# Optimization experiments

Measured on AMD Instinct MI355X. Metric: run time of the kernel, lower is better.

The kernel has to match this reference:

```python
import jax, jax.numpy as jnp
import numpy as np

BS, T, D_IN = 128, 32, 128
DH = 128          # controller hidden size == memory word width M
N_SLOTS = 512     # memory rows
EPS = 1e-8


def _split_read(o):
    # o: [bs, M+6] -> k, beta, g, s(3), gamma
    k = o[:, :DH]
    beta = jax.nn.softplus(o[:, DH])
    g = jax.nn.sigmoid(o[:, DH + 1])
    s = jax.nn.softmax(o[:, DH + 2:DH + 5], axis=-1)
    gamma = 1.0 + jax.nn.softplus(o[:, DH + 5])
    return k, beta, g, s, gamma


def _attention(k, beta, g, s, gamma, mem, w_prev):
    # content addressing: cosine similarity sharpened by beta
    dot = jnp.einsum('bnm,bm->bn', mem, k)
    denom = jnp.linalg.norm(mem, axis=-1) * jnp.linalg.norm(k, axis=-1, keepdims=True) + EPS
    w_c = jax.nn.softmax(beta[:, None] * dot / denom, axis=-1)
    # gate interpolation with previous weights
    w_g = g[:, None] * w_c + (1.0 - g[:, None]) * w_prev
    # circular shift convolution over offsets {-1, 0, +1}
    w_t = (s[:, 0:1] * jnp.roll(w_g, -1, axis=-1)
           + s[:, 1:2] * w_g
           + s[:, 2:3] * jnp.roll(w_g, 1, axis=-1))
    # sharpening
    w = w_t ** gamma[:, None]
    return w / (jnp.sum(w, axis=-1, keepdims=True) + EPS)


def setup_inputs() -> dict:
    key = jax.random.key(0)
    ks = jax.random.split(key, 8)
    sc = lambda fan_in: 1.0 / np.sqrt(fan_in)
    return {
        'x':    jax.random.normal(ks[0], (BS, T, D_IN), jnp.float32),
        'Wxh':  jax.random.normal(ks[1], (D_IN, DH), jnp.float32) * sc(D_IN),
        'Whh':  jax.random.normal(ks[2], (DH, DH), jnp.float32) * sc(DH),
        'Wrh':  jax.random.normal(ks[3], (DH, DH), jnp.float32) * sc(DH),
        'bh':   jnp.zeros((DH,), jnp.float32),
        'Wout': jax.random.normal(ks[4], (DH + DH, D_IN), jnp.float32) * sc(2 * DH),
        'bout': jnp.zeros((D_IN,), jnp.float32),
        'Wr':   jax.random.normal(ks[5], (DH, DH + 6), jnp.float32) * sc(DH),
        'br':   jnp.zeros((DH + 6,), jnp.float32),
        'Ww':   jax.random.normal(ks[6], (DH, 3 * DH + 6), jnp.float32) * sc(DH),
        'bw':   jnp.zeros((3 * DH + 6,), jnp.float32),
    }


def reference(x, Wxh, Whh, Wrh, bh, Wout, bout, Wr, br, Ww, bw):
    bs = x.shape[0]
    h0 = jnp.zeros((bs, DH), x.dtype)
    r0 = jnp.zeros((bs, DH), x.dtype)
    w0 = jnp.full((bs, N_SLOTS), 1.0 / N_SLOTS, x.dtype)
    mem0 = jnp.full((bs, N_SLOTS, DH), 1e-6, x.dtype)

    def step(carry, x_t):
        h, r, w_prev, mem = carry
        # controller state
        h = jnp.tanh(x_t @ Wxh + h @ Whh + r @ Wrh + bh)
        # head parameter projections
        o_r = h @ Wr + br
        o_w = h @ Ww + bw
        k_r, b_r, g_r, s_r, y_r = _split_read(o_r)
        k_w, b_w_, g_w, s_w, y_w = _split_read(o_w[:, :DH + 6])
        e = jax.nn.sigmoid(o_w[:, DH + 6:2 * DH + 6])   # erase [bs, M]
        a = jnp.tanh(o_w[:, 2 * DH + 6:3 * DH + 6])     # add   [bs, M]
        # addressing (w_previous updated sequentially, read then write)
        w_r = _attention(k_r, b_r, g_r, s_r, y_r, mem, w_prev)
        w_w = _attention(k_w, b_w_, g_w, s_w, y_w, mem, w_r)
        # read
        r = jnp.einsum('bn,bnm->bm', w_r, mem)
        # erase / add write
        mem = mem * (1.0 - w_w[:, :, None] * e[:, None, :]) + w_w[:, :, None] * a[:, None, :]
        # output
        y = jnp.concatenate([h, r], axis=-1) @ Wout + bout
        return (h, r, w_w, mem), y

    _, ys = jax.lax.scan(step, (h0, r0, w0, mem0), jnp.swapaxes(x, 0, 1))
    return jnp.swapaxes(ys, 0, 1)  # [bs, ft, d_output]
```

## Files before the change

kernel.cpp:

```cpp
#include <hip/hip_runtime.h>
#include <hip/hip_bf16.h>
#include <math.h>

#define NT 1024
#define BSZ 128
#define TSTEPS 32
#define DIN 128
#define DHH 128
#define NSLOT 512
#define EPSF 1e-8f

static constexpr int F_FLOATS = 7160;
static constexpr size_t LDS_BYTES = 131072 + F_FLOATS * sizeof(float);

__device__ __forceinline__ float bf_lo(unsigned u) {
  union { unsigned u; float f; } c; c.u = u << 16; return c.f;
}
__device__ __forceinline__ float bf_hi(unsigned u) {
  union { unsigned u; float f; } c; c.u = u & 0xffff0000u; return c.f;
}
__device__ __forceinline__ unsigned short f2us(float f) {
  union { unsigned short s; __hip_bfloat16 h; } c; c.h = __float2bfloat16(f); return c.s;
}
__device__ __forceinline__ unsigned pkbf(float a, float b) {
  union { __hip_bfloat162 h2; unsigned u; } c;
  c.h2 = __float22bfloat162_rn(make_float2(a, b));
  return c.u;
}
__device__ __forceinline__ float sigmoid_(float x) { return 1.0f / (1.0f + __expf(-x)); }
__device__ __forceinline__ float softplus_(float x) {
  return fmaxf(x, 0.0f) + log1pf(__expf(-fabsf(x)));
}
__device__ __forceinline__ float tanh_(float x) {
  float e = __expf(-2.0f * fabsf(x));
  float t = (1.0f - e) / (1.0f + e);
  return copysignf(t, x);
}
__device__ __forceinline__ float waveSum(float v) {
#pragma unroll
  for (int m = 32; m >= 1; m >>= 1) v += __shfl_xor(v, m);
  return v;
}

__global__ __launch_bounds__(NT, 4)
void ntm_kernel(const float* __restrict__ x,
                const float* __restrict__ Wxh,
                const float* __restrict__ Whh,
                const float* __restrict__ Wrh,
                const float* __restrict__ bh,
                const float* __restrict__ Wout,
                const float* __restrict__ bout,
                const float* __restrict__ Wr,
                const float* __restrict__ br,
                const float* __restrict__ Ww,
                const float* __restrict__ bw,
                float* __restrict__ out)
{
  extern __shared__ char smem[];
  uint4* memv = (uint4*)smem;
  float* F = (float*)(smem + 131072);

  const int b = blockIdx.x;
  const int tid = threadIdx.x;
  const int g = tid >> 4, l = tid & 15;
  const int lane = tid & 63, wid = tid >> 6;

  float* U      = F + 0;
  float* yP     = F + 2560;
  float* sWprev = F + 4608;
  float* sWr    = F + 5120;
  float* sP1    = F + 5632;
  float* sOr    = F + 6144;
  float* sOw    = F + 6288;
  float* sH     = F + 6680;
  float* sR     = F + 6808;
  float* sXt    = F + 6936;
  float* sP     = F + 7064;
  uint4* krP    = (uint4*)(sP1 + 0);
  uint4* kwP    = (uint4*)(sP1 + 64);
  float* eR     = U + 0;
  float* eW     = U + 512;

  {
    const unsigned short mb = f2us(1e-6f);
    const unsigned w32 = ((unsigned)mb << 16) | mb;
    const uint4 fv = make_uint4(w32, w32, w32, w32);
    for (int i = tid; i < NSLOT * DHH / 8; i += NT) memv[i] = fv;
  }
  for (int i = tid; i < NSLOT; i += NT) sWprev[i] = 1.0f / NSLOT;
  if (tid < DHH) { sH[tid] = 0.0f; sR[tid] = 0.0f; }
  if (tid < DIN) sXt[tid] = x[(size_t)b * TSTEPS * DIN + tid];
  __syncthreads();

  for (int t = 0; t < TSTEPS; ++t) {
    {
      if (t > 0 && tid < DIN) {
        float y = bout[tid];
#pragma unroll
        for (int q = 0; q < 16; ++q) y += yP[q * 128 + tid];
        out[((size_t)b * TSTEPS + (t - 1)) * DIN + tid] = y;
      }
      const int q = tid & 63, s = tid >> 6;
      const int j2 = q * 2, i0 = s * 24;
      float2 acc = make_float2(0.f, 0.f);
#pragma unroll 8
      for (int w = 0; w < 24; ++w) {
        const int i = i0 + w;
        float v; const float* Wp;
        if (i < 128)      { v = sXt[i];       Wp = Wxh + i * DHH; }
        else if (i < 256) { v = sH[i - 128];  Wp = Whh + (i - 128) * DHH; }
        else              { v = sR[i - 256];  Wp = Wrh + (i - 256) * DHH; }
        const float2 wv = *(const float2*)(Wp + j2);
        acc.x = fmaf(v, wv.x, acc.x);
        acc.y = fmaf(v, wv.y, acc.y);
      }
      *(float2*)(U + s * 128 + j2) = acc;
      __syncthreads();
    }
    if (tid < DHH) {
      float a2 = bh[tid];
#pragma unroll
      for (int q2 = 0; q2 < 16; ++q2) a2 += U[q2 * 128 + tid];
      sH[tid] = tanh_(a2);
    }
    __syncthreads();

    {
#pragma unroll
      for (int k = 0; k < 2; ++k) {
        const int s = tid + k * NT;
        if (s < 1048) {
          const int q = (s >= 786) ? 3 : (s >= 524) ? 2 : (s >= 262) ? 1 : 0;
          const int P = s - 262 * q;
          const float2* p;
          int strideF2;
          if (P < 67) { p = (const float2*)(Wr + 32 * q * 134 + 2 * P); strideF2 = 67; }
          else        { p = (const float2*)(Ww + 32 * q * 390 + 2 * (P - 67)); strideF2 = 195; }
          const int i0 = 32 * q;
          float2 acc = make_float2(0.f, 0.f);
#pragma unroll 8
          for (int w = 0; w < 32; ++w) {
            const float v = sH[i0 + w];
            const float2 wv = *p;
            acc.x = fmaf(v, wv.x, acc.x);
            acc.y = fmaf(v, wv.y, acc.y);
            p += strideF2;
          }
          *(float2*)(U + s * 2) = acc;
        }
      }
      __syncthreads();
    }
    if (tid < 524) {
      float v = 0.f;
#pragma unroll
      for (int q = 0; q < 4; ++q) v += U[tid + 524 * q];
      if (tid < 134) sOr[tid] = v + br[tid];
      else {
        const int cw = tid - 134;
        sOw[(cw < 134) ? cw : cw + 2] = v + bw[cw];
      }
    }
    __syncthreads();
    {
      if (wid < 4) {
        float v = (tid < 128) ? sOr[tid] * sOr[tid] : sOw[tid - 128] * sOw[tid - 128];
        v = waveSum(v);
        if (lane == 0) sP[wid] = v;
      } else if (tid >= 256 && tid < 384) {
        const int q = tid - 256; sOw[136 + q] = sigmoid_(sOw[136 + q]);
      } else if (tid >= 384 && tid < 512) {
        const int q = tid - 384; sOw[264 + q] = tanh_(sOw[264 + q]);
      } else if (tid >= 512 && tid < 544) {
        const int t2 = tid - 512;
        const int c = t2 & 15;
        const float* src = (t2 < 16) ? (sOr + c * 8) : (sOw + c * 8);
        union { uint4 v; unsigned short h[8]; } pk;
#pragma unroll
        for (int j = 0; j < 8; ++j) pk.h[j] = f2us(src[j]);
        if (t2 < 16) krP[c] = pk.v; else kwP[c] = pk.v;
      } else if (tid == 544) {
        sP[80] = softplus_(sOr[128]);
        sP[81] = sigmoid_(sOr[129]);
        float a0 = sOr[130], a1 = sOr[131], a2 = sOr[132];
        float mx = fmaxf(a0, fmaxf(a1, a2));
        float e0 = __expf(a0 - mx), e1 = __expf(a1 - mx), e2 = __expf(a2 - mx);
        float es = e0 + e1 + e2;
        sP[82] = e0 / es; sP[83] = e1 / es; sP[84] = e2 / es;
        sP[85] = 1.0f + softplus_(sOr[133]);
      } else if (tid == 545) {
        sP[86] = softplus_(sOw[128]);
        sP[87] = sigmoid_(sOw[129]);
        float a0 = sOw[130], a1 = sOw[131], a2 = sOw[132];
        float mx = fmaxf(a0, fmaxf(a1, a2));
        float e0 = __expf(a0 - mx), e1 = __expf(a1 - mx), e2 = __expf(a2 - mx);
        float es = e0 + e1 + e2;
        sP[88] = e0 / es; sP[89] = e1 / es; sP[90] = e2 / es;
        sP[91] = 1.0f + softplus_(sOw[133]);
      }
      __syncthreads();
    }

    {
      const float kn_r = sqrtf(sP[0] + sP[1]);
      const float kn_w = sqrtf(sP[2] + sP[3]);
      const float beta_r = sP[80], beta_w = sP[86];
      const int n = tid >> 1, hf = tid & 1;
      const int sw = (n >> 2) & 3;
      float dr = 0.f, dw = 0.f, ss = 0.f;
#pragma unroll
      for (int c = 0; c < 8; ++c) {
        const int cl = hf * 8 + c;
        const uint4 mv = memv[n * 16 + (cl ^ sw)];
        const uint4 kr = krP[cl];
        const uint4 kw = kwP[cl];
        const unsigned mw_[4] = { mv.x, mv.y, mv.z, mv.w };
        const unsigned krw[4] = { kr.x, kr.y, kr.z, kr.w };
        const unsigned kww[4] = { kw.x, kw.y, kw.z, kw.w };
#pragma unroll
        for (int j = 0; j < 4; ++j) {
          const float m0 = bf_lo(mw_[j]), m1 = bf_hi(mw_[j]);
          dr = fmaf(m0, bf_lo(krw[j]), dr); dr = fmaf(m1, bf_hi(krw[j]), dr);
          dw = fmaf(m0, bf_lo(kww[j]), dw); dw = fmaf(m1, bf_hi(kww[j]), dw);
          ss = fmaf(m0, m0, ss);            ss = fmaf(m1, m1, ss);
        }
      }
      dr += __shfl_xor(dr, 1);
      dw += __shfl_xor(dw, 1);
      ss += __shfl_xor(ss, 1);
      const float nr = sqrtf(ss);
      const float er = __expf(beta_r * dr / (nr * kn_r + EPSF));
      const float ew = __expf(beta_w * dw / (nr * kn_w + EPSF));
      if (hf == 0) { eR[n] = er; eW[n] = ew; }
      float s1 = waveSum(er) * 0.5f;
      float s2 = waveSum(ew) * 0.5f;
      if (lane == 0) { sP[16 + wid] = s1; sP[32 + wid] = s2; }
      __syncthreads();
    }

    {
      float p1 = 0.0f;
      if (tid < NSLOT) {
        float SR = 0.f;
#pragma unroll
        for (int q = 0; q < 16; ++q) SR += sP[16 + q];
        const float invE = 1.0f / SR;
        const float gr = sP[81], omg = 1.0f - sP[81];
        const int im = (tid - 1) & 511, ip = (tid + 1) & 511;
        const float wgm = gr * (eR[im] * invE) + omg * sWprev[im];
        const float wg0 = gr * (eR[tid] * invE) + omg * sWprev[tid];
        const float wgp = gr * (eR[ip] * invE) + omg * sWprev[ip];
        const float wt = sP[82] * wgp + sP[83] * wg0 + sP[84] * wgm;
        p1 = (wt > 0.0f) ? __expf(sP[85] * __logf(wt)) : 0.0f;
      }
      float P = waveSum(p1);
      if (tid < NSLOT) sP1[tid] = p1;
      if (lane == 0) sP[48 + wid] = P;
      __syncthreads();
    }
    {
      float p2 = 0.0f;
      if (tid < NSLOT) {
        float PS = 0.f, SW = 0.f;
#pragma unroll
        for (int q = 0; q < 16; ++q) { PS += sP[48 + q]; SW += sP[32 + q]; }
        const float pinv1 = 1.0f / (PS + EPSF);
        const float invE = 1.0f / SW;
        const float gw = sP[87], omg = 1.0f - sP[87];
        const int im = (tid - 1) & 511, ip = (tid + 1) & 511;
        const float wgm = gw * (eW[im] * invE) + omg * (sP1[im] * pinv1);
        const float wg0 = gw * (eW[tid] * invE) + omg * (sP1[tid] * pinv1);
        const float wgp = gw * (eW[ip] * invE) + omg * (sP1[ip] * pinv1);
        sWr[tid] = sP1[tid] * pinv1;
        const float wt = sP[88] * wgp + sP[89] * wg0 + sP[90] * wgm;
        p2 = (wt > 0.0f) ? __expf(sP[91] * __logf(wt)) : 0.0f;
      }
      float P = waveSum(p2);
      if (tid < NSLOT) U[tid] = p2;
      if (lane == 0) sP[64 + wid] = P;
      __syncthreads();
    }

    {
      float PS = 0.f;
#pragma unroll
      for (int q = 0; q < 16; ++q) PS += sP[64 + q];
      const float pinv2 = 1.0f / (PS + EPSF);
      if (tid < NSLOT) sWprev[tid] = U[tid] * pinv2;

      const int cl = l ^ ((g >> 2) & 3);
      float4 e4a = *(const float4*)(sOw + 136 + cl * 8);
      float4 e4b = *(const float4*)(sOw + 140 + cl * 8);
      float4 a4a = *(const float4*)(sOw + 264 + cl * 8);
      float4 a4b = *(const float4*)(sOw + 268 + cl * 8);
      const float e8[8] = { e4a.x, e4a.y, e4a.z, e4a.w, e4b.x, e4b.y, e4b.z, e4b.w };
      const float a8[8] = { a4a.x, a4a.y, a4a.z, a4a.w, a4b.x, a4b.y, a4b.z, a4b.w };
      float r8[8] = { 0, 0, 0, 0, 0, 0, 0, 0 };
#pragma unroll 2
      for (int it = 0; it < 8; ++it) {
        const int n = g + 64 * it;
        const float wrn = sWr[n];
        const float wwn = U[n] * pinv2;
        uint4 pk = memv[n * 16 + l];
        const unsigned wds[4] = { pk.x, pk.y, pk.z, pk.w };
        float m[8];
#pragma unroll
        for (int j = 0; j < 4; ++j) { m[2 * j] = bf_lo(wds[j]); m[2 * j + 1] = bf_hi(wds[j]); }
#pragma unroll
        for (int j = 0; j < 8; ++j) {
          r8[j] = fmaf(wrn, m[j], r8[j]);
          const float d = fmaf(-e8[j], m[j], a8[j]);
          m[j] = fmaf(wwn, d, m[j]);
        }
        pk.x = pkbf(m[0], m[1]);
        pk.y = pkbf(m[2], m[3]);
        pk.z = pkbf(m[4], m[5]);
        pk.w = pkbf(m[6], m[7]);
        memv[n * 16 + l] = pk;
      }
#pragma unroll
      for (int j = 0; j < 8; ++j) {
        r8[j] += __shfl_xor(r8[j], 16);
        r8[j] += __shfl_xor(r8[j], 32);
      }
      if (lane < 16) {
        *(float4*)(U + 512 + wid * 128 + cl * 8)     = make_float4(r8[0], r8[1], r8[2], r8[3]);
        *(float4*)(U + 512 + wid * 128 + cl * 8 + 4) = make_float4(r8[4], r8[5], r8[6], r8[7]);
      }
      __syncthreads();
    }
    if (tid < DHH) {
      float acc = 0.0f;
#pragma unroll
      for (int q = 0; q < 16; ++q) acc += U[512 + q * 128 + tid];
      sR[tid] = acc;
    }
    __syncthreads();

    {
      if (tid >= 896 && t + 1 < TSTEPS) {
        const int i = tid - 896;
        sXt[i] = x[((size_t)b * TSTEPS + (t + 1)) * DIN + i];
      }
      if (tid < 512) {
        const int q = tid & 31, s = tid >> 5;
        const int j4 = q * 4, i0 = s * 16;
        float4 acc = make_float4(0.f, 0.f, 0.f, 0.f);
#pragma unroll
        for (int i = i0; i < i0 + 16; ++i) {
          const float v = (i < 128) ? sH[i] : sR[i - 128];
          const float4 w = *(const float4*)(Wout + i * DIN + j4);
          acc.x = fmaf(v, w.x, acc.x); acc.y = fmaf(v, w.y, acc.y);
          acc.z = fmaf(v, w.z, acc.z); acc.w = fmaf(v, w.w, acc.w);
        }
        *(float4*)(yP + s * 128 + j4) = acc;
      }
      __syncthreads();
    }
  }

  if (tid < DIN) {
    float y = bout[tid];
#pragma unroll
    for (int q = 0; q < 16; ++q) y += yP[q * 128 + tid];
    out[((size_t)b * TSTEPS + (TSTEPS - 1)) * DIN + tid] = y;
  }
}

extern "C" void kernel_launch(void* const* d_in, const int* in_sizes, int n_in,
                              void* d_out, int out_size, void* d_ws, size_t ws_size,
                              hipStream_t stream) {
  (void)in_sizes; (void)n_in; (void)out_size; (void)d_ws; (void)ws_size;
  hipFuncSetAttribute(reinterpret_cast<const void*>(ntm_kernel),
                      hipFuncAttributeMaxDynamicSharedMemorySize, (int)LDS_BYTES);
  ntm_kernel<<<dim3(BSZ), dim3(NT), LDS_BYTES, stream>>>(
      (const float*)d_in[0], (const float*)d_in[1], (const float*)d_in[2],
      (const float*)d_in[3], (const float*)d_in[4], (const float*)d_in[5],
      (const float*)d_in[6], (const float*)d_in[7], (const float*)d_in[8],
      (const float*)d_in[9], (const float*)d_in[10],
      (float*)d_out);
}
```

Before: 964.3 us.

## Merge addressing phases with LDS atomics and overlap output projection with idle threads

After: 1.422 ms. 1.47x slower.

```diff
diff --git a/kernel.cpp b/kernel.cpp
--- a/kernel.cpp
+++ b/kernel.cpp
@@ -72,9 +72,7 @@
   float* sP1    = F + 5632;
   float* sOr    = F + 6144;
   float* sOw    = F + 6288;
-  float* sH     = F + 6680;
-  float* sR     = F + 6808;
-  float* sXt    = F + 6936;
+  float* X      = F + 6680;
   float* sP     = F + 7064;
   uint4* krP    = (uint4*)(sP1 + 0);
   uint4* kwP    = (uint4*)(sP1 + 64);
@@ -88,8 +86,7 @@
     for (int i = tid; i < NSLOT * DHH / 8; i += NT) memv[i] = fv;
   }
   for (int i = tid; i < NSLOT; i += NT) sWprev[i] = 1.0f / NSLOT;
-  if (tid < DHH) { sH[tid] = 0.0f; sR[tid] = 0.0f; }
-  if (tid < DIN) sXt[tid] = x[(size_t)b * TSTEPS * DIN + tid];
+  if (tid < 384) X[tid] = (tid < 128) ? x[(size_t)b * TSTEPS * DIN + tid] : 0.0f;
   __syncthreads();
 
   for (int t = 0; t < TSTEPS; ++t) {
@@ -102,17 +99,21 @@
       }
       const int q = tid & 63, s = tid >> 6;
       const int j2 = q * 2, i0 = s * 24;
+      union { float4 v4[6]; float f[24]; } xv;
+      const float4* Xp = (const float4*)(X + i0);
+#pragma unroll
+      for (int j = 0; j < 6; ++j) xv.v4[j] = Xp[j];
       float2 acc = make_float2(0.f, 0.f);
-#pragma unroll 8
+#pragma unroll
       for (int w = 0; w < 24; ++w) {
         const int i = i0 + w;
-        float v; const float* Wp;
-        if (i < 128)      { v = sXt[i];       Wp = Wxh + i * DHH; }
-        else if (i < 256) { v = sH[i - 128];  Wp = Whh + (i - 128) * DHH; }
-        else              { v = sR[i - 256];  Wp = Wrh + (i - 256) * DHH; }
+        const float* Wp;
+        if (i < 128)      Wp = Wxh + i * DHH;
+        else if (i < 256) Wp = Whh + (i - 128) * DHH;
+        else              Wp = Wrh + (i - 256) * DHH;
         const float2 wv = *(const float2*)(Wp + j2);
-        acc.x = fmaf(v, wv.x, acc.x);
-        acc.y = fmaf(v, wv.y, acc.y);
+        acc.x = fmaf(xv.f[w], wv.x, acc.x);
+        acc.y = fmaf(xv.f[w], wv.y, acc.y);
       }
       *(float2*)(U + s * 128 + j2) = acc;
       __syncthreads();
@@ -121,7 +122,7 @@
       float a2 = bh[tid];
 #pragma unroll
       for (int q2 = 0; q2 < 16; ++q2) a2 += U[q2 * 128 + tid];
-      sH[tid] = tanh_(a2);
+      X[128 + tid] = tanh_(a2);
     }
     __syncthreads();
 
@@ -132,18 +133,20 @@
         if (s < 1048) {
           const int q = (s >= 786) ? 3 : (s >= 524) ? 2 : (s >= 262) ? 1 : 0;
           const int P = s - 262 * q;
+          union { float4 v4[8]; float f[32]; } hq;
+          const float4* Hp = (const float4*)(X + 128 + 32 * q);
+#pragma unroll
+          for (int j = 0; j < 8; ++j) hq.v4[j] = Hp[j];
           const float2* p;
           int strideF2;
           if (P < 67) { p = (const float2*)(Wr + 32 * q * 134 + 2 * P); strideF2 = 67; }
           else        { p = (const float2*)(Ww + 32 * q * 390 + 2 * (P - 67)); strideF2 = 195; }
-          const int i0 = 32 * q;
           float2 acc = make_float2(0.f, 0.f);
 #pragma unroll 8
           for (int w = 0; w < 32; ++w) {
-            const float v = sH[i0 + w];
             const float2 wv = *p;
-            acc.x = fmaf(v, wv.x, acc.x);
-            acc.y = fmaf(v, wv.y, acc.y);
+            acc.x = fmaf(hq.f[w], wv.x, acc.x);
+            acc.y = fmaf(hq.f[w], wv.y, acc.y);
             p += strideF2;
           }
           *(float2*)(U + s * 2) = acc;
@@ -160,13 +163,15 @@
         const int cw = tid - 134;
         sOw[(cw < 134) ? cw : cw + 2] = v + bw[cw];
       }
+    } else if (tid == 1000) {
+      sP[0] = 0.f; sP[1] = 0.f; sP[2] = 0.f; sP[3] = 0.f; sP[4] = 0.f; sP[5] = 0.f;
     }
     __syncthreads();
     {
       if (wid < 4) {
         float v = (tid < 128) ? sOr[tid] * sOr[tid] : sOw[tid - 128] * sOw[tid - 128];
         v = waveSum(v);
-        if (lane == 0) sP[wid] = v;
+        if (lane == 0) atomicAdd(&sP[wid >> 1], v);
       } else if (tid >= 256 && tid < 384) {
         const int q = tid - 256; sOw[136 + q] = sigmoid_(sOw[136 + q]);
       } else if (tid >= 384 && tid < 512) {
@@ -202,8 +207,8 @@
     }
 
     {
-      const float kn_r = sqrtf(sP[0] + sP[1]);
-      const float kn_w = sqrtf(sP[2] + sP[3]);
+      const float kn_r = sqrtf(sP[0]);
+      const float kn_w = sqrtf(sP[1]);
       const float beta_r = sP[80], beta_w = sP[86];
       const int n = tid >> 1, hf = tid & 1;
       const int sw = (n >> 2) & 3;
@@ -234,38 +239,45 @@
       if (hf == 0) { eR[n] = er; eW[n] = ew; }
       float s1 = waveSum(er) * 0.5f;
       float s2 = waveSum(ew) * 0.5f;
-      if (lane == 0) { sP[16 + wid] = s1; sP[32 + wid] = s2; }
-      __syncthreads();
-    }
-
-    {
-      float p1 = 0.0f;
+      if (lane == 0) { atomicAdd(&sP[2], s1); atomicAdd(&sP[3], s2); }
+      __syncthreads();
+    }
+
+    {
       if (tid < NSLOT) {
-        float SR = 0.f;
-#pragma unroll
-        for (int q = 0; q < 16; ++q) SR += sP[16 + q];
-        const float invE = 1.0f / SR;
+        const float invE = 1.0f / sP[2];
         const float gr = sP[81], omg = 1.0f - sP[81];
         const int im = (tid - 1) & 511, ip = (tid + 1) & 511;
         const float wgm = gr * (eR[im] * invE) + omg * sWprev[im];
         const float wg0 = gr * (eR[tid] * invE) + omg * sWprev[tid];
         const float wgp = gr * (eR[ip] * invE) + omg * sWprev[ip];
         const float wt = sP[82] * wgp + sP[83] * wg0 + sP[84] * wgm;
-        p1 = (wt > 0.0f) ? __expf(sP[85] * __logf(wt)) : 0.0f;
-      }
-      float P = waveSum(p1);
-      if (tid < NSLOT) sP1[tid] = p1;
-      if (lane == 0) sP[48 + wid] = P;
-      __syncthreads();
-    }
-    {
-      float p2 = 0.0f;
+        float p1 = (wt > 0.0f) ? __expf(sP[85] * __logf(wt)) : 0.0f;
+        float P = waveSum(p1);
+        sP1[tid] = p1;
+        if (lane == 0) atomicAdd(&sP[4], P);
+      } else {
+        const int p = tid - 512;
+        const int j4 = (p & 31) * 4, sl = p >> 5;
+        union { float4 v4[2]; float f[8]; } hv;
+        const float4* Hp = (const float4*)(X + 128 + 8 * sl);
+        hv.v4[0] = Hp[0]; hv.v4[1] = Hp[1];
+        float4 acc = make_float4(0.f, 0.f, 0.f, 0.f);
+#pragma unroll
+        for (int w = 0; w < 8; ++w) {
+          const float4 wv = *(const float4*)(Wout + (8 * sl + w) * DIN + j4);
+          const float v = hv.f[w];
+          acc.x = fmaf(v, wv.x, acc.x); acc.y = fmaf(v, wv.y, acc.y);
+          acc.z = fmaf(v, wv.z, acc.z); acc.w = fmaf(v, wv.w, acc.w);
+        }
+        *(float4*)(yP + sl * 128 + j4) = acc;
+      }
+      __syncthreads();
+    }
+    {
       if (tid < NSLOT) {
-        float PS = 0.f, SW = 0.f;
-#pragma unroll
-        for (int q = 0; q < 16; ++q) { PS += sP[48 + q]; SW += sP[32 + q]; }
-        const float pinv1 = 1.0f / (PS + EPSF);
-        const float invE = 1.0f / SW;
+        const float pinv1 = 1.0f / (sP[4] + EPSF);
+        const float invE = 1.0f / sP[3];
         const float gw = sP[87], omg = 1.0f - sP[87];
         const int im = (tid - 1) & 511, ip = (tid + 1) & 511;
         const float wgm = gw * (eW[im] * invE) + omg * (sP1[im] * pinv1);
@@ -273,19 +285,19 @@
         const float wgp = gw * (eW[ip] * invE) + omg * (sP1[ip] * pinv1);
         sWr[tid] = sP1[tid] * pinv1;
         const float wt = sP[88] * wgp + sP[89] * wg0 + sP[90] * wgm;
-        p2 = (wt > 0.0f) ? __expf(sP[91] * __logf(wt)) : 0.0f;
-      }
-      float P = waveSum(p2);
-      if (tid < NSLOT) U[tid] = p2;
-      if (lane == 0) sP[64 + wid] = P;
-      __syncthreads();
-    }
-
-    {
-      float PS = 0.f;
-#pragma unroll
-      for (int q = 0; q < 16; ++q) PS += sP[64 + q];
-      const float pinv2 = 1.0f / (PS + EPSF);
+        float p2 = (wt > 0.0f) ? __expf(sP[91] * __logf(wt)) : 0.0f;
+        float P = waveSum(p2);
+        U[tid] = p2;
+        if (lane == 0) atomicAdd(&sP[5], P);
+      } else if (tid < 512 + DIN && t + 1 < TSTEPS) {
+        const int i = tid - 512;
+        X[i] = x[((size_t)b * TSTEPS + (t + 1)) * DIN + i];
+      }
+      __syncthreads();
+    }
+
+    {
+      const float pinv2 = 1.0f / (sP[5] + EPSF);
       if (tid < NSLOT) sWprev[tid] = U[tid] * pinv2;
 
       const int cl = l ^ ((g >> 2) & 3);
@@ -333,27 +345,25 @@
       float acc = 0.0f;
 #pragma unroll
       for (int q = 0; q < 16; ++q) acc += U[512 + q * 128 + tid];
-      sR[tid] = acc;
+      X[256 + tid] = acc;
     }
     __syncthreads();
 
     {
-      if (tid >= 896 && t + 1 < TSTEPS) {
-        const int i = tid - 896;
-        sXt[i] = x[((size_t)b * TSTEPS + (t + 1)) * DIN + i];
-      }
       if (tid < 512) {
-        const int q = tid & 31, s = tid >> 5;
-        const int j4 = q * 4, i0 = s * 16;
-        float4 acc = make_float4(0.f, 0.f, 0.f, 0.f);
-#pragma unroll
-        for (int i = i0; i < i0 + 16; ++i) {
-          const float v = (i < 128) ? sH[i] : sR[i - 128];
-          const float4 w = *(const float4*)(Wout + i * DIN + j4);
-          acc.x = fmaf(v, w.x, acc.x); acc.y = fmaf(v, w.y, acc.y);
-          acc.z = fmaf(v, w.z, acc.z); acc.w = fmaf(v, w.w, acc.w);
-        }
-        *(float4*)(yP + s * 128 + j4) = acc;
+        const int j4 = (tid & 31) * 4, sl = tid >> 5;
+        union { float4 v4[2]; float f[8]; } rv;
+        const float4* Rp = (const float4*)(X + 256 + 8 * sl);
+        rv.v4[0] = Rp[0]; rv.v4[1] = Rp[1];
+        float4 acc = *(const float4*)(yP + sl * 128 + j4);
+#pragma unroll
+        for (int w = 0; w < 8; ++w) {
+          const float4 wv = *(const float4*)(Wout + (128 + 8 * sl + w) * DIN + j4);
+          const float v = rv.f[w];
+          acc.x = fmaf(v, wv.x, acc.x); acc.y = fmaf(v, wv.y, acc.y);
+          acc.z = fmaf(v, wv.z, acc.z); acc.w = fmaf(v, wv.w, acc.w);
+        }
+        *(float4*)(yP + sl * 128 + j4) = acc;
       }
       __syncthreads();
     }
```
